# Kernel optimization log

Hardware: AMD Instinct MI355X
Metric: run time of the kernel (lower is better)

## Reference

```python
import jax, jax.numpy as jnp
import numpy as np

N_LAYERS, B, S, D, H, DH = 4, 4, 512, 512, 8, 64
MEM, CMEM, RATIO, FFMUL, VOCAB, LLAT = 512, 128, 4, 4, 512, 256
KV = CMEM + MEM + S  # 1152


def layernorm(x, g, b, eps=1e-5):
    mu = x.mean(-1, keepdims=True)
    var = ((x - mu) ** 2).mean(-1, keepdims=True)
    return (x - mu) * jax.lax.rsqrt(var + eps) * g + b


def shift(x):
    # Music-Transformer skewing: x [..., i, j] -> relative-shifted [..., i, j]
    *lead, i, j = x.shape
    x = jnp.concatenate([x, jnp.zeros((*lead, i, i), x.dtype)], -1)
    l = i + j - 1
    x = x.reshape(*lead, i * (i + j))
    pad = (-x.shape[-1]) % l
    x = jnp.concatenate([x, jnp.zeros((*lead, pad), x.dtype)], -1)
    x = x.reshape(*lead, -1, l)
    return x[..., :i, i - 1:]


def full_attn(q, k, v, mask=None, pos_emb=None):
    dh = q.shape[-1]
    dots = jnp.einsum('bhid,bhjd->bhij', q, k) * (dh ** -0.5)
    if pos_emb is not None:
        pos_dots = jnp.einsum('bhid,hjd->bhij', q, pos_emb) * (dh ** 0.5)
        pos_dots = shift(pos_dots)[..., :dots.shape[-1]]
        dots = dots + pos_dots
    if mask is not None:
        dots = jnp.where(mask, dots, jnp.asarray(-1e9, dots.dtype))
    attn = jax.nn.softmax(dots, -1)
    return jnp.einsum('bhij,bhjd->bhid', attn, v), attn


def heads(x):
    b, n, _ = x.shape
    return x.reshape(b, n, H, DH).transpose(0, 2, 1, 3)


def mha(q_in, k_in, v_in, W, mask=None, pos_emb=None):
    # W: [4, D, D] (q, k, v, out), applied as x @ W
    q, k, v = heads(q_in @ W[0]), heads(k_in @ W[1]), heads(v_in @ W[2])
    x, w = full_attn(q, k, v, mask=mask, pos_emb=pos_emb)
    x = x.transpose(0, 2, 1, 3).reshape(q_in.shape[0], -1, D)
    return x @ W[3], w


def conv_compress(mem, w, b):
    # Conv1d(D, D, RATIO, stride=RATIO): kernel==stride -> block reshape
    Bb, L, _ = mem.shape
    m = mem.reshape(Bb, L // RATIO, RATIO, D)
    return jnp.einsum('blrd,odr->blo', m, w) + b


def forward(trg, trg_mask, src_mask, latent, mems, cmems, pos_emb, embed,
            W_self, ln1_g, ln1_b, conv_w, conv_b, W_src, ln2_g, ln2_b,
            w1, b1, w2, b2):
    x = jnp.take(embed, trg, axis=0)  # [B, S, D]
    tm = trg_mask[:, :, None] & trg_mask[:, None, :]  # [B, S, S]
    tm = jnp.pad(tm, ((0, 0), (0, 0), (CMEM + MEM, 0)), constant_values=True)[:, None]  # [B,1,S,KV]
    sm = src_mask[:, None]  # [B, 1, S, LLAT]
    sg = jax.lax.stop_gradient
    attn_loss = jnp.asarray(0.0, jnp.float32)
    for i in range(N_LAYERS):
        m, cm = mems[i], cmems[i]
        kv = jnp.concatenate([cm, m, x], 1)  # [B, KV, D]
        a, _ = mha(x, kv, kv, W_self[i], mask=tm, pos_emb=pos_emb)
        a = layernorm(a + x, ln1_g[i], ln1_b[i])
        old_mem = m[:, :S]
        new_cm = conv_compress(old_mem, conv_w[i], conv_b[i])  # [B, S//RATIO, D]
        x = a
        # reconstruction attention loss: detached h / weights / old_mem
        Wq, Wk, Wv = sg(W_self[i, 0]), sg(W_self[i, 1]), sg(W_self[i, 2])
        hs = sg(x)

        def rattn(mm):
            q, k, v = heads(hs @ Wq), heads(mm @ Wk), heads(mm @ Wv)
            return full_attn(q, k, v)[0]

        target = sg(rattn(sg(old_mem)))
        attn_loss = attn_loss + jnp.mean((rattn(new_cm) - target) ** 2)
        # cross attention to latent
        x, _ = mha(x, latent, latent, W_src[i], mask=sm)
        # residual pre-norm feed-forward (GELU, exact erf as nn.GELU)
        y = layernorm(x, ln2_g[i], ln2_b[i])
        x = x + jax.nn.gelu(y @ w1[i] + b1[i], approximate=False) @ w2[i] + b2[i]
    return x, attn_loss / N_LAYERS


def setup_inputs() -> dict:
    key = jax.random.key(0)
    ks = jax.random.split(key, 16)
    sc = 0.02
    return {
        'trg': jax.random.randint(ks[0], (B, S), 0, VOCAB, dtype=jnp.int32),
        'trg_mask': jnp.ones((B, S), dtype=bool),
        'src_mask': jnp.ones((B, S, LLAT), dtype=bool),
        'latent': jax.random.normal(ks[1], (B, LLAT, D), jnp.float32),
        'mems': jax.random.normal(ks[2], (N_LAYERS, B, MEM, D), jnp.float32) * sc,
        'cmems': jax.random.normal(ks[3], (N_LAYERS, B, CMEM, D), jnp.float32) * sc,
        'pos_emb': jax.random.normal(ks[4], (H, KV, DH), jnp.float32) * sc,
        'embed': jax.random.normal(ks[5], (VOCAB, D), jnp.float32) * sc,
        'W_self': jax.random.normal(ks[6], (N_LAYERS, 4, D, D), jnp.float32) * sc,
        'ln1_g': jnp.ones((N_LAYERS, D), jnp.float32),
        'ln1_b': jnp.zeros((N_LAYERS, D), jnp.float32),
        'conv_w': jax.random.normal(ks[7], (N_LAYERS, D, D, RATIO), jnp.float32) * sc,
        'conv_b': jnp.zeros((N_LAYERS, D), jnp.float32),
        'W_src': jax.random.normal(ks[8], (N_LAYERS, 4, D, D), jnp.float32) * sc,
        'ln2_g': jnp.ones((N_LAYERS, D), jnp.float32),
        'ln2_b': jnp.zeros((N_LAYERS, D), jnp.float32),
        'w1': jax.random.normal(ks[9], (N_LAYERS, D, D * FFMUL), jnp.float32) * sc,
        'b1': jnp.zeros((N_LAYERS, D * FFMUL), jnp.float32),
        'w2': jax.random.normal(ks[10], (N_LAYERS, D * FFMUL, D), jnp.float32) * sc,
        'b2': jnp.zeros((N_LAYERS, D), jnp.float32),
    }


def reference(trg, trg_mask, src_mask, latent, mems, cmems, pos_emb, embed,
              W_self, ln1_g, ln1_b, conv_w, conv_b, W_src, ln2_g, ln2_b,
              w1, b1, w2, b2):
    return forward(trg, trg_mask, src_mask, latent, mems, cmems, pos_emb, embed,
                   W_self, ln1_g, ln1_b, conv_w, conv_b, W_src, ln2_g, ln2_b,
                   w1, b1, w2, b2)
```

## Files before the change

kernel.cpp:

```cpp
#include <hip/hip_runtime.h>
#include <math.h>

typedef float floatx4 __attribute__((ext_vector_type(4)));
typedef __bf16 bf16x8 __attribute__((ext_vector_type(8)));
typedef unsigned short u16;

#define LDK 72

__device__ inline u16 to_bf16(float f) {
  union { float f; unsigned u; } v; v.f = f;
  unsigned u = v.u;
  u += 0x7FFFu + ((u >> 16) & 1u);
  return (u16)(u >> 16);
}
__device__ inline float bf2f(u16 h) {
  union { unsigned u; float f; } v; v.u = ((unsigned)h) << 16; return v.f;
}

__device__ inline void gload16(const void* g, void* l) {
  __builtin_amdgcn_global_load_lds(
      (const __attribute__((address_space(1))) unsigned int*)g,
      (__attribute__((address_space(3))) unsigned int*)l, 16, 0, 0);
}

struct GemmArgs {
  const void* A; const void* B; void* C;
  int lda, ldb, ldc, N, Kc;
  long sA1, sA2, sB1, sB2, sC1, sC2;
  float alpha;
  const float* bias;
  const float* res; int ldres;
  const float* aml;
  int amode;
  int cmode;
  int act;
  int smode;
  int bdiv, kparts;
  int gx, gy;
};

#define MAXG 10
struct GemmBatch {
  GemmArgs g[MAXG];
  int end[MAXG];
  int ng;
};

__global__ __launch_bounds__(256) void gemmb_k(GemmBatch gb) {
  int bid = blockIdx.x;
  int gi = 0;
  while (bid >= gb.end[gi]) ++gi;
  const GemmArgs g = gb.g[gi];
  int lb = bid - (gi ? gb.end[gi - 1] : 0);
  int tid = threadIdx.x;

  if (g.amode == 8) {
    long i = (long)lb * 1024 + tid * 4;
    const float* bs = g.bias;
    int bi = (int)(i & 511);
    float4 r = *(const float4*)(g.res + i);
    float4 v;
    v.x = r.x + bs[bi]; v.y = r.y + bs[bi + 1];
    v.z = r.z + bs[bi + 2]; v.w = r.w + bs[bi + 3];
    *(float4*)((float*)g.C + i) = v;
    return;
  }
  if (g.amode == 9) {
    const float* oc = (const float*)g.A;
    const float* Op = (const float*)g.B;
    const float* ml = g.aml;
    float s = 0.f;
    for (long i = (long)lb * 256 + tid; i < 1048576; i += 256L * g.gx) {
      int row = (int)(i >> 9), col = (int)(i & 511), h = col >> 6;
      const float* mlp = ml + ((long)row * 8 + h) * 2;
      float m0v = mlp[0], l0v = mlp[1];
      float m1v = mlp[32768], l1v = mlp[32769];
      float mm = fmaxf(m0v, m1v);
      float w0 = __expf(m0v - mm), w1 = __expf(m1v - mm);
      float ov = (w0 * Op[i] + w1 * Op[1048576 + i]) / (w0 * l0v + w1 * l1v);
      float d = oc[i] - ov; s += d * d;
    }
    for (int o = 32; o > 0; o >>= 1) s += __shfl_xor(s, o, 64);
    __shared__ float red[4];
    if ((tid & 63) == 0) red[tid >> 6] = s;
    __syncthreads();
    if (tid == 0) atomicAdd((float*)g.C, red[0] + red[1] + red[2] + red[3]);
    return;
  }

  int bx = lb % g.gx;
  int rem = lb / g.gx;
  int by = rem % g.gy;
  int z = rem / g.gy;

  int kp = z % g.kparts;
  int zz = z / g.kparts;
  int zi = zz / g.bdiv, zj = zz % g.bdiv;
  long aoff = (long)zi * g.sA1 + (long)zj * g.sA2;
  long boff = (long)zi * g.sB1 + (long)zj * g.sB2;
  long coff = (long)zi * g.sC1 + (long)zj * g.sC2;
  const float* Af = (const float*)g.A + aoff;
  const u16* Ah = (const u16*)g.A + aoff;
  const u16* Bh = (const u16*)g.B + boff;

  int m0 = by * 64, n0 = bx * 64;
  __shared__ u16 As[64][64];
  __shared__ u16 Bs[64][64];
  char* Asb = (char*)&As[0][0];
  char* Bsb = (char*)&Bs[0][0];
  int wave = tid >> 6, lane = tid & 63;
  int wr = (wave >> 1) * 32, wc = (wave & 1) * 32;
  int lr = lane & 15, qrow = lane >> 4;

  unsigned o0 = wave * 1024u + lane * 16u;
  unsigned o1 = o0 + 4096u;
  int ga_r0 = o0 >> 7, ga_r1 = o1 >> 7;
  int ga_c0 = (int)(o0 & 127u) ^ ((ga_r0 & 7) << 4);
  int ga_c1 = (int)(o1 & 127u) ^ ((ga_r1 & 7) << 4);
  long ldaB = (long)g.lda * 2, ldbB = (long)g.ldb * 2;
  int r = tid >> 2, c16 = (tid & 3) << 4;
  int sw0 = (r << 7) + (((tid & 3) << 5) ^ ((r & 7) << 4));
  int sw1 = (r << 7) + ((((tid & 3) << 5) + 16) ^ ((r & 7) << 4));

  floatx4 acc[2][2];
#pragma unroll
  for (int i = 0; i < 2; ++i)
#pragma unroll
    for (int j = 0; j < 2; ++j)
#pragma unroll
      for (int rr = 0; rr < 4; ++rr) acc[i][j][rr] = 0.f;

  int kb0 = kp * g.Kc, kb1 = kb0 + g.Kc;
  for (int k0 = kb0; k0 < kb1; k0 += 64) {
    if (g.amode == 1) {
      const char* Ab = (const char*)Ah + ((long)m0 * g.lda + k0) * 2;
      gload16(Ab + ga_r0 * ldaB + ga_c0, Asb + wave * 1024);
      gload16(Ab + ga_r1 * ldaB + ga_c1, Asb + 4096 + wave * 1024);
    } else if (g.amode == 0) {
      const float* ap = Af + (long)(m0 + r) * g.lda + k0 + c16;
      float4 a0 = *(const float4*)ap, a1 = *(const float4*)(ap + 4);
      float4 a2 = *(const float4*)(ap + 8), a3 = *(const float4*)(ap + 12);
      union { u16 s[8]; uint4 v; } u0, u1;
      u0.s[0] = to_bf16(a0.x); u0.s[1] = to_bf16(a0.y); u0.s[2] = to_bf16(a0.z); u0.s[3] = to_bf16(a0.w);
      u0.s[4] = to_bf16(a1.x); u0.s[5] = to_bf16(a1.y); u0.s[6] = to_bf16(a1.z); u0.s[7] = to_bf16(a1.w);
      u1.s[0] = to_bf16(a2.x); u1.s[1] = to_bf16(a2.y); u1.s[2] = to_bf16(a2.z); u1.s[3] = to_bf16(a2.w);
      u1.s[4] = to_bf16(a3.x); u1.s[5] = to_bf16(a3.y); u1.s[6] = to_bf16(a3.z); u1.s[7] = to_bf16(a3.w);
      *(uint4*)(Asb + sw0) = u0.v; *(uint4*)(Asb + sw1) = u1.v;
    } else {
      int row = m0 + r;
      int k = k0 + c16;
      int ns = g.N;
      const float* mlp = g.aml + ((long)row * 8 + (k >> 6)) * 2;
      float mm = -1e30f;
#pragma unroll 3
      for (int s = 0; s < 3; ++s)
        if (s < ns) mm = fmaxf(mm, mlp[s * 32768]);
      float wgt[3]; float den = 0.f;
#pragma unroll 3
      for (int s = 0; s < 3; ++s)
        if (s < ns) { wgt[s] = __expf(mlp[s * 32768] - mm); den += wgt[s] * mlp[s * 32768 + 1]; }
      float inv = 1.f / den;
      float a16[16];
#pragma unroll
      for (int j = 0; j < 16; ++j) a16[j] = 0.f;
      const float* p0 = (const float*)g.A + (long)row * g.lda + k;
#pragma unroll 3
      for (int s = 0; s < 3; ++s)
        if (s < ns) {
          float w = wgt[s] * inv;
          const float* p = p0 + (long)s * g.sA1;
#pragma unroll
          for (int j = 0; j < 4; ++j) {
            float4 xx = *(const float4*)(p + j * 4);
            a16[j * 4 + 0] += w * xx.x; a16[j * 4 + 1] += w * xx.y;
            a16[j * 4 + 2] += w * xx.z; a16[j * 4 + 3] += w * xx.w;
          }
        }
      union { u16 s[8]; uint4 v; } u0, u1;
#pragma unroll
      for (int j = 0; j < 8; ++j) u0.s[j] = to_bf16(a16[j]);
#pragma unroll
      for (int j = 0; j < 8; ++j) u1.s[j] = to_bf16(a16[8 + j]);
      *(uint4*)(Asb + sw0) = u0.v; *(uint4*)(Asb + sw1) = u1.v;
    }
    {
      const char* Bb = (const char*)Bh + ((long)n0 * g.ldb + k0) * 2;
      gload16(Bb + ga_r0 * ldbB + ga_c0, Bsb + wave * 1024);
      gload16(Bb + ga_r1 * ldbB + ga_c1, Bsb + 4096 + wave * 1024);
    }
    __syncthreads();
#pragma unroll
    for (int ks = 0; ks < 2; ++ks) {
      int xk = ((ks * 32 + qrow * 8) << 1) ^ ((lr & 7) << 4);
      int rA0 = wr + lr, rB0 = wc + lr;
      bf16x8 a0 = *(const bf16x8*)(Asb + (rA0 << 7) + xk);
      bf16x8 a1 = *(const bf16x8*)(Asb + ((rA0 + 16) << 7) + xk);
      bf16x8 b0 = *(const bf16x8*)(Bsb + (rB0 << 7) + xk);
      bf16x8 b1 = *(const bf16x8*)(Bsb + ((rB0 + 16) << 7) + xk);
      acc[0][0] = __builtin_amdgcn_mfma_f32_16x16x32_bf16(a0, b0, acc[0][0], 0, 0, 0);
      acc[0][1] = __builtin_amdgcn_mfma_f32_16x16x32_bf16(a0, b1, acc[0][1], 0, 0, 0);
      acc[1][0] = __builtin_amdgcn_mfma_f32_16x16x32_bf16(a1, b0, acc[1][0], 0, 0, 0);
      acc[1][1] = __builtin_amdgcn_mfma_f32_16x16x32_bf16(a1, b1, acc[1][1], 0, 0, 0);
    }
    __syncthreads();
  }

#pragma unroll
  for (int mt = 0; mt < 2; ++mt)
#pragma unroll
    for (int nt = 0; nt < 2; ++nt) {
      int row0 = m0 + wr + mt * 16 + qrow * 4;
      int col = n0 + wc + nt * 16 + lr;
      if (g.cmode == 2) {
        ushort4 o;
        o.x = to_bf16(acc[mt][nt][0] * g.alpha);
        o.y = to_bf16(acc[mt][nt][1] * g.alpha);
        o.z = to_bf16(acc[mt][nt][2] * g.alpha);
        o.w = to_bf16(acc[mt][nt][3] * g.alpha);
        *(ushort4*)((u16*)g.C + coff + (long)col * g.ldc + row0) = o;
      } else {
#pragma unroll
        for (int rr = 0; rr < 4; ++rr) {
          int row = row0 + rr;
          float v = acc[mt][nt][rr] * g.alpha;
          if (g.cmode == 3) {
            atomicAdd((float*)g.C + coff + (long)row * g.ldc + col, v);
          } else if (g.smode) {
            int oc = col + row - 511;
            if (oc >= 0) ((u16*)g.C + coff)[(long)row * g.ldc + oc] = to_bf16(v);
          } else {
            if (g.bias) v += g.bias[col];
            if (g.res) v += g.res[(long)row * g.ldres + col];
            if (g.act) v = 0.5f * v * (1.0f + erff(v * 0.70710678118654752f));
            if (g.cmode == 1) ((u16*)g.C + coff)[(long)row * g.ldc + col] = to_bf16(v);
            else ((float*)g.C + coff)[(long)row * g.ldc + col] = v;
          }
        }
      }
    }
}

struct FAttnArgs {
  const u16* Q; const u16* K; const u16* V; const u16* QP;
  void* O; float* Opart; float* ml;
  int L, nsplit; long sKb, sVb; int ldV;
  float scale; int obf16;
};

struct FBatch {
  FAttnArgs a[3];
  int zend[3];
  int nf;
};

__global__ __launch_bounds__(256) void fattnb_k(FBatch fb) {
  int zg = blockIdx.z;
  int fi = 0;
  while (zg >= fb.zend[fi]) ++fi;
  const FAttnArgs a = fb.a[fi];
  int zl = zg - (fi ? fb.zend[fi - 1] : 0);

  int qt = blockIdx.x, h = blockIdx.y;
  int b = zl / a.nsplit, sp = zl % a.nsplit;
  int Lc = a.L / a.nsplit, kt0 = sp * Lc, T = Lc >> 6;
  int tid = threadIdx.x, wave = tid >> 6, lane = tid & 63;
  int lr = lane & 15, quad = lane >> 4;
  __shared__ u16 Qs[64][LDK];
  __shared__ u16 Ks[2][64][LDK];
  __shared__ u16 Vs[2][64][LDK];
  __shared__ u16 Qp[4][16][LDK];
  __shared__ u16 Ps[4][16][LDK];
  int r = tid >> 2, c = (tid & 3) << 4;
  {
    const u16* qp = a.Q + (long)(b * 512 + qt * 64 + r) * 512 + h * 64 + c;
    *(uint4*)&Qs[r][c] = *(const uint4*)qp;
    *(uint4*)&Qs[r][c + 8] = *(const uint4*)(qp + 8);
  }
  const u16* Kb = a.K + (long)b * a.sKb + h * 64;
  const u16* Vb = a.V + (long)b * a.sVb + (long)(h * 64) * a.ldV;
  int qrow16 = lane >> 2, qc = (lane & 3) << 4;
  const u16* QPr = a.QP ? a.QP + ((long)b * 8 + h) * 589824 +
                          (long)(qt * 64 + wave * 16 + qrow16) * 1152 : nullptr;
  {
    const u16* kp = Kb + (long)(kt0 + r) * 512 + c;
    *(uint4*)&Ks[0][r][c] = *(const uint4*)kp;
    *(uint4*)&Ks[0][r][c + 8] = *(const uint4*)(kp + 8);
    const u16* vp = Vb + (long)r * a.ldV + kt0 + c;
    *(uint4*)&Vs[0][r][c] = *(const uint4*)vp;
    *(uint4*)&Vs[0][r][c + 8] = *(const uint4*)(vp + 8);
  }
  uint4 qpr0, qpr1;
  if (QPr) {
    qpr0 = *(const uint4*)(QPr + kt0 + qc);
    qpr1 = *(const uint4*)(QPr + kt0 + qc + 8);
  }

  float m_run[4], l_run[4];
  floatx4 oacc[4];
#pragma unroll
  for (int i = 0; i < 4; ++i) {
    m_run[i] = -1e30f; l_run[i] = 0.f;
#pragma unroll
    for (int j = 0; j < 4; ++j) oacc[i][j] = 0.f;
  }

  for (int t = 0; t < T; ++t) {
    int cur = t & 1;
    bool more = (t + 1) < T;
    __syncthreads();
    uint4 pk0, pk1, pv0, pv1;
    if (more) {
      int kt = kt0 + (t + 1) * 64;
      const u16* kp = Kb + (long)(kt + r) * 512 + c;
      pk0 = *(const uint4*)kp; pk1 = *(const uint4*)(kp + 8);
      const u16* vp = Vb + (long)r * a.ldV + kt + c;
      pv0 = *(const uint4*)vp; pv1 = *(const uint4*)(vp + 8);
    }
    floatx4 sacc[4];
#pragma unroll
    for (int nt = 0; nt < 4; ++nt)
#pragma unroll
      for (int j = 0; j < 4; ++j) sacc[nt][j] = 0.f;
#pragma unroll
    for (int ks = 0; ks < 2; ++ks) {
      int kq = ks * 32 + quad * 8;
      bf16x8 av = *(const bf16x8*)&Qs[wave * 16 + lr][kq];
#pragma unroll
      for (int nt = 0; nt < 4; ++nt) {
        bf16x8 bb = *(const bf16x8*)&Ks[cur][nt * 16 + lr][kq];
        sacc[nt] = __builtin_amdgcn_mfma_f32_16x16x32_bf16(av, bb, sacc[nt], 0, 0, 0);
      }
    }
    if (QPr) {
      *(uint4*)&Qp[wave][qrow16][qc] = qpr0;
      *(uint4*)&Qp[wave][qrow16][qc + 8] = qpr1;
#pragma unroll
      for (int nt = 0; nt < 4; ++nt)
#pragma unroll
        for (int rr = 0; rr < 4; ++rr)
          sacc[nt][rr] = sacc[nt][rr] * a.scale + bf2f(Qp[wave][quad * 4 + rr][nt * 16 + lr]);
      if (more) {
        qpr0 = *(const uint4*)(QPr + kt0 + (t + 1) * 64 + qc);
        qpr1 = *(const uint4*)(QPr + kt0 + (t + 1) * 64 + qc + 8);
      }
    } else {
#pragma unroll
      for (int nt = 0; nt < 4; ++nt)
#pragma unroll
        for (int rr = 0; rr < 4; ++rr) sacc[nt][rr] *= a.scale;
    }
#pragma unroll
    for (int rr = 0; rr < 4; ++rr) {
      float m = -1e30f;
#pragma unroll
      for (int nt = 0; nt < 4; ++nt) m = fmaxf(m, sacc[nt][rr]);
      for (int o = 8; o > 0; o >>= 1) m = fmaxf(m, __shfl_xor(m, o, 64));
      float mn = fmaxf(m_run[rr], m);
      float al = __expf(m_run[rr] - mn);
      m_run[rr] = mn;
      float s = 0.f;
#pragma unroll
      for (int nt = 0; nt < 4; ++nt) {
        float p = __expf(sacc[nt][rr] - mn);
        sacc[nt][rr] = p;
        s += p;
      }
      for (int o = 8; o > 0; o >>= 1) s += __shfl_xor(s, o, 64);
      l_run[rr] = l_run[rr] * al + s;
#pragma unroll
      for (int nt = 0; nt < 4; ++nt) oacc[nt][rr] *= al;
    }
#pragma unroll
    for (int nt = 0; nt < 4; ++nt) {
      Ps[wave][quad * 4 + 0][nt * 16 + lr] = to_bf16(sacc[nt][0]);
      Ps[wave][quad * 4 + 1][nt * 16 + lr] = to_bf16(sacc[nt][1]);
      Ps[wave][quad * 4 + 2][nt * 16 + lr] = to_bf16(sacc[nt][2]);
      Ps[wave][quad * 4 + 3][nt * 16 + lr] = to_bf16(sacc[nt][3]);
    }
#pragma unroll
    for (int ks = 0; ks < 2; ++ks) {
      int kq = ks * 32 + quad * 8;
      bf16x8 av = *(const bf16x8*)&Ps[wave][lr][kq];
#pragma unroll
      for (int nt = 0; nt < 4; ++nt) {
        bf16x8 bb = *(const bf16x8*)&Vs[cur][nt * 16 + lr][kq];
        oacc[nt] = __builtin_amdgcn_mfma_f32_16x16x32_bf16(av, bb, oacc[nt], 0, 0, 0);
      }
    }
    if (more) {
      *(uint4*)&Ks[cur ^ 1][r][c] = pk0; *(uint4*)&Ks[cur ^ 1][r][c + 8] = pk1;
      *(uint4*)&Vs[cur ^ 1][r][c] = pv0; *(uint4*)&Vs[cur ^ 1][r][c + 8] = pv1;
    }
  }
  if (a.nsplit == 1) {
    float inv[4];
#pragma unroll
    for (int rr = 0; rr < 4; ++rr) inv[rr] = 1.f / l_run[rr];
#pragma unroll
    for (int nt = 0; nt < 4; ++nt)
#pragma unroll
      for (int rr = 0; rr < 4; ++rr) {
        long row = b * 512 + qt * 64 + wave * 16 + quad * 4 + rr;
        float v = oacc[nt][rr] * inv[rr];
        if (a.obf16) ((u16*)a.O)[row * 512 + h * 64 + nt * 16 + lr] = to_bf16(v);
        else ((float*)a.O)[row * 512 + h * 64 + nt * 16 + lr] = v;
      }
  } else {
#pragma unroll
    for (int nt = 0; nt < 4; ++nt)
#pragma unroll
      for (int rr = 0; rr < 4; ++rr) {
        long row = b * 512 + qt * 64 + wave * 16 + quad * 4 + rr;
        a.Opart[((long)sp * 2048 + row) * 512 + h * 64 + nt * 16 + lr] = oacc[nt][rr];
      }
    if (lr == 0)
#pragma unroll
      for (int rr = 0; rr < 4; ++rr) {
        long row = b * 512 + qt * 64 + wave * 16 + quad * 4 + rr;
        long mi = (((long)sp * 2048 + row) * 8 + h) * 2;
        a.ml[mi] = m_run[rr]; a.ml[mi + 1] = l_run[rr];
      }
  }
}

struct PrepArgs { const void* a; const void* b; void* c; int mode, p0, p1, gx, gy; };
struct PrepBatch { PrepArgs p[10]; int end[10]; int np; };

__global__ __launch_bounds__(256) void prep_k(PrepBatch pb) {
  int bid = blockIdx.x, gi = 0;
  while (bid >= pb.end[gi]) ++gi;
  PrepArgs p = pb.p[gi];
  int lb = bid - (gi ? pb.end[gi - 1] : 0);
  int tid = threadIdx.x;
  __shared__ float t[32][33];
  if (p.mode == 0) {
    int i = lb * 256 + tid;
    int row = i >> 9, d = i & 511;
    ((float*)p.c)[i] = ((const float*)p.a)[(long)((const int*)p.b)[row] * 512 + d];
  } else if (p.mode == 1) {
    int K = p.p0, N = p.p1;
    int bx = lb % p.gx, by = (lb / p.gx) % p.gy, z = lb / (p.gx * p.gy);
    const float* in = (const float*)p.a + (long)z * K * N;
    u16* out = (u16*)p.c + (long)z * K * N;
    int n0 = bx * 32, k0 = by * 32;
    int tx = tid & 31, ty = tid >> 5;
    for (int j = 0; j < 32; j += 8) t[ty + j][tx] = in[(long)(k0 + ty + j) * N + n0 + tx];
    __syncthreads();
    for (int j = 0; j < 32; j += 8) out[(long)(n0 + ty + j) * K + k0 + tx] = to_bf16(t[tx][ty + j]);
  } else if (p.mode == 2) {
    int z = lb >> 12; int i = (lb & 4095) * 256 + tid;
    int o = i >> 11, k = i & 2047, r2 = k >> 9, d = k & 511;
    ((u16*)p.c)[(long)z * 1048576 + i] =
        to_bf16(((const float*)p.a)[(long)z * 1048576 + o * 2048 + d * 4 + r2]);
  } else if (p.mode == 3) {
    int i = lb * 256 + tid;
    if (i < p.p0) ((u16*)p.c)[i] = to_bf16(((const float*)p.a)[i]);
  } else if (p.mode == 4) {
    int i = lb * 256 + tid;
    ((float*)p.c)[i] = ((const float*)p.a)[((i >> 18) << 9) + (i & 511)];
  } else {
    int i = lb * 256 + tid;
    if (i < p.p0) { uint4 z4 = {0, 0, 0, 0}; ((uint4*)p.c)[i] = z4; }
  }
}

__global__ __launch_bounds__(256) void layernorm_k(const float* __restrict__ X,
                                                   const float* __restrict__ g,
                                                   const float* __restrict__ b,
                                                   u16* __restrict__ Y) {
  long row = blockIdx.x;
  const float* x = X + row * 512;
  int tid = threadIdx.x;
  float v0 = x[tid], v1 = x[tid + 256];
  __shared__ float red[256];
  red[tid] = v0 + v1; __syncthreads();
  for (int o = 128; o > 0; o >>= 1) { if (tid < o) red[tid] += red[tid + o]; __syncthreads(); }
  float mu = red[0] * (1.f / 512.f);
  __syncthreads();
  float d0 = v0 - mu, d1 = v1 - mu;
  red[tid] = d0 * d0 + d1 * d1; __syncthreads();
  for (int o = 128; o > 0; o >>= 1) { if (tid < o) red[tid] += red[tid + o]; __syncthreads(); }
  float rstd = rsqrtf(red[0] * (1.f / 512.f) + 1e-5f);
  Y[row * 512 + tid] = to_bf16(d0 * rstd * g[tid] + b[tid]);
  Y[row * 512 + tid + 256] = to_bf16(d1 * rstd * g[tid + 256] + b[tid + 256]);
}

__global__ __launch_bounds__(256) void finalize_k(const float* __restrict__ x,
                                                  const float* __restrict__ loss,
                                                  float* __restrict__ out) {
  long i = (long)blockIdx.x * 256 + threadIdx.x;
  if (i < 1048576) out[i] = x[i];
  else if (i == 1048576) out[i] = loss[0] * (1.f / (1048576.f * 4.f));
}

extern "C" void kernel_launch(void* const* d_in, const int* in_sizes, int n_in,
                              void* d_out, int out_size, void* d_ws, size_t ws_size,
                              hipStream_t stream) {
  (void)in_sizes; (void)n_in; (void)out_size;
  const int* trg = (const int*)d_in[0];
  const float* latent = (const float*)d_in[3];
  const float* mems = (const float*)d_in[4];
  const float* cmems = (const float*)d_in[5];
  const float* pos_emb = (const float*)d_in[6];
  const float* embed = (const float*)d_in[7];
  const float* W_self = (const float*)d_in[8];
  const float* ln1_g = (const float*)d_in[9];
  const float* ln1_b = (const float*)d_in[10];
  const float* conv_w = (const float*)d_in[11];
  const float* conv_b = (const float*)d_in[12];
  const float* W_src = (const float*)d_in[13];
  const float* ln2_g = (const float*)d_in[14];
  const float* ln2_b = (const float*)d_in[15];
  const float* w1 = (const float*)d_in[16];
  const float* b1 = (const float*)d_in[17];
  const float* w2 = (const float*)d_in[18];
  const float* b2 = (const float*)d_in[19];

  float* ws = (float*)d_ws;
  long off = 0;
  auto alloc = [&](long n) { float* p = ws + off; off += (n + 63) & ~63L; return p; };
  float* x    = alloc(1048576);
  float* t0   = alloc(1048576);
  float* t1   = alloc(1048576);
  float* ocm  = alloc(1048576);
  float* Opart= alloc(3145728);
  float* mlb  = alloc(98304);
  float* Opart2 = alloc(2097152);
  u16* h1   = (u16*)Opart2;
  float* mlb2 = alloc(65536);
  u16* qb   = (u16*)alloc(524288);
  u16* qc   = (u16*)alloc(524288);
  u16* xa   = (u16*)alloc(524288);
  u16* t1h  = (u16*)alloc(524288);
  u16* kbuf = (u16*)alloc(1179648);
  u16* vbuf = (u16*)alloc(1179648);
  u16* kcm4 = (u16*)alloc(524288);
  u16* vcm4 = (u16*)alloc(524288);
  u16* klat4= (u16*)alloc(1048576);
  u16* vlat4= (u16*)alloc(1048576);
  float* ncm4 = alloc(1048576);
  u16* SQP  = (u16*)alloc(9437184);
  u16* wts  = (u16*)alloc(2097152);
  u16* wsr  = (u16*)alloc(2097152);
  u16* w1t  = (u16*)alloc(2097152);
  u16* w2t  = (u16*)alloc(2097152);
  u16* cwt  = (u16*)alloc(2097152);
  u16* post = (u16*)alloc(294912);
  float* lossacc = alloc(64);
  if ((size_t)off * 4 > ws_size) return;

  PrepBatch PB; PB.np = 0; int ptot = 0;
  auto padd = [&](int mode, const void* a, const void* b, void* c,
                  int p0, int p1, int gx, int gy, int blocks) {
    PrepArgs pa; pa.a = a; pa.b = b; pa.c = c; pa.mode = mode;
    pa.p0 = p0; pa.p1 = p1; pa.gx = gx; pa.gy = gy;
    PB.p[PB.np] = pa; ptot += blocks; PB.end[PB.np] = ptot; PB.np++;
  };
  padd(0, embed, trg, x, 0, 0, 0, 0, 4096);
  padd(1, W_self, nullptr, wts, 512, 512, 16, 16, 4096);
  padd(1, W_src, nullptr, wsr, 512, 512, 16, 16, 4096);
  padd(1, w1, nullptr, w1t, 512, 2048, 64, 16, 4096);
  padd(1, w2, nullptr, w2t, 2048, 512, 16, 64, 4096);
  padd(2, conv_w, nullptr, cwt, 0, 0, 0, 0, 16384);
  padd(3, pos_emb, nullptr, post, 589824, 0, 0, 0, 2304);
  padd(4, conv_b, nullptr, ncm4, 0, 0, 0, 0, 4096);
  padd(5, nullptr, nullptr, SQP, 2359296, 0, 0, 0, 9216);
  padd(5, nullptr, nullptr, lossacc, 1, 0, 0, 0, 1);
  prep_k<<<dim3(ptot), 256, 0, stream>>>(PB);

  auto ga = []() { GemmArgs g; g.alpha = 1.f; g.bias = nullptr; g.res = nullptr; g.ldres = 512;
                   g.aml = nullptr;
                   g.amode = 0; g.cmode = 0; g.act = 0; g.smode = 0; g.bdiv = 1; g.kparts = 1;
                   g.sA1 = g.sA2 = g.sB1 = g.sB2 = g.sC1 = g.sC2 = 0; g.N = 0;
                   g.gx = g.gy = 1; return g; };
  GemmBatch GB; GB.ng = 0; int gtot = 0;
  auto badd = [&](GemmArgs g, int gx, int gy, int gz) {
    g.gx = gx; g.gy = gy;
    GB.g[GB.ng] = g; gtot += gx * gy * gz; GB.end[GB.ng] = gtot; GB.ng++;
  };
  auto brun = [&]() {
    gemmb_k<<<dim3(gtot), 256, 0, stream>>>(GB);
    GB.ng = 0; gtot = 0;
  };
  auto run1 = [&](GemmArgs g, int gx, int gy, int gz) { badd(g, gx, gy, gz); brun(); };

  FBatch FB; FB.nf = 0; int ztot = 0;
  auto fadd = [&](const u16* Q, const u16* K, const u16* V, const u16* QP, void* O,
                  int L, int nsplit, long sKb, long sVb, int ldV, int obf16,
                  float* Op, float* ml) {
    FAttnArgs a; a.Q = Q; a.K = K; a.V = V; a.QP = QP; a.O = O;
    a.Opart = Op; a.ml = ml;
    a.L = L; a.nsplit = nsplit; a.sKb = sKb; a.sVb = sVb; a.ldV = ldV;
    a.scale = 0.125f; a.obf16 = obf16;
    FB.a[FB.nf] = a; ztot += 4 * nsplit; FB.zend[FB.nf] = ztot; FB.nf++;
  };
  auto frun = [&]() {
    fattnb_k<<<dim3(8, 8, ztot), 256, 0, stream>>>(FB);
    FB.nf = 0; ztot = 0;
  };

  { GemmArgs g = ga(); g.A = latent; g.lda = 512; g.B = wsr + 262144; g.ldb = 512;
    g.sB1 = 1048576; g.C = klat4; g.ldc = 512; g.sC1 = 524288; g.cmode = 1; g.Kc = 512;
    badd(g, 8, 16, 4); }
  { GemmArgs g = ga(); g.A = latent; g.lda = 512; g.B = wsr + 2 * 262144; g.ldb = 512;
    g.sB1 = 1048576; g.C = vlat4; g.ldc = 1024; g.sC1 = 524288; g.cmode = 2; g.Kc = 512;
    badd(g, 8, 16, 4); }
  { GemmArgs g = ga(); g.A = mems; g.lda = 2048; g.sA1 = 1048576;
    g.B = cwt; g.ldb = 2048; g.sB1 = 1048576;
    g.C = ncm4; g.ldc = 512; g.sC1 = 262144; g.cmode = 3; g.kparts = 8; g.Kc = 256;
    badd(g, 8, 8, 32); }
  brun();

  for (int l = 0; l < 4; ++l) {
    const u16* Wt0 = wts + (l * 4 + 0) * 262144;
    const u16* Wt1 = wts + (l * 4 + 1) * 262144;
    const u16* Wt2 = wts + (l * 4 + 2) * 262144;
    const u16* Wt3 = wts + (l * 4 + 3) * 262144;
    const u16* Ws0 = wsr + (l * 4 + 0) * 262144;
    const u16* Ws3 = wsr + (l * 4 + 3) * 262144;
    const float* mem_l = mems + (long)l * 1048576;
    const float* cmem_l = cmems + (long)l * 262144;
    const u16* kcm_l = kcm4 + (long)l * 262144;
    const u16* vcm_l = vcm4 + (long)l * 262144;
    const u16* klat_l = klat4 + (long)l * 524288;
    const u16* vlat_l = vlat4 + (long)l * 524288;

    { GemmArgs g = ga(); g.A = x; g.lda = 512; g.B = Wt0; g.ldb = 512; g.C = qb; g.ldc = 512;
      g.cmode = 1; g.Kc = 512; badd(g, 8, 32, 1); }
    { GemmArgs g = ga(); g.A = cmem_l; g.lda = 512; g.sA1 = 65536; g.B = Wt1; g.ldb = 512;
      g.C = kbuf; g.ldc = 512; g.sC1 = 589824; g.cmode = 1; g.Kc = 512; badd(g, 8, 2, 4); }
    { GemmArgs g = ga(); g.A = mem_l; g.lda = 512; g.sA1 = 262144; g.B = Wt1; g.ldb = 512;
      g.C = kbuf + 128 * 512; g.ldc = 512; g.sC1 = 589824; g.cmode = 1; g.Kc = 512;
      badd(g, 8, 8, 4); }
    { GemmArgs g = ga(); g.A = x; g.lda = 512; g.sA1 = 262144; g.B = Wt1; g.ldb = 512;
      g.C = kbuf + 640 * 512; g.ldc = 512; g.sC1 = 589824; g.cmode = 1; g.Kc = 512;
      badd(g, 8, 8, 4); }
    { GemmArgs g = ga(); g.A = cmem_l; g.lda = 512; g.sA1 = 65536; g.B = Wt2; g.ldb = 512;
      g.C = vbuf; g.ldc = 1152; g.sC1 = 589824; g.cmode = 2; g.Kc = 512; badd(g, 8, 2, 4); }
    { GemmArgs g = ga(); g.A = mem_l; g.lda = 512; g.sA1 = 262144; g.B = Wt2; g.ldb = 512;
      g.C = vbuf + 128; g.ldc = 1152; g.sC1 = 589824; g.cmode = 2; g.Kc = 512;
      badd(g, 8, 8, 4); }
    { GemmArgs g = ga(); g.A = x; g.lda = 512; g.sA1 = 262144; g.B = Wt2; g.ldb = 512;
      g.C = vbuf + 640; g.ldc = 1152; g.sC1 = 589824; g.cmode = 2; g.Kc = 512;
      badd(g, 8, 8, 4); }
    if (l == 0) {
      { GemmArgs g = ga(); g.A = ncm4; g.lda = 512; g.sA1 = 262144; g.B = wts + 262144;
        g.ldb = 512; g.sB1 = 1048576; g.C = kcm4; g.ldc = 512; g.sC1 = 262144;
        g.cmode = 1; g.Kc = 512; badd(g, 8, 8, 4); }
      { GemmArgs g = ga(); g.A = ncm4; g.lda = 512; g.sA1 = 262144; g.B = wts + 2 * 262144;
        g.ldb = 512; g.sB1 = 1048576; g.C = vcm4; g.ldc = 512; g.sC1 = 262144;
        g.cmode = 2; g.Kc = 512; badd(g, 8, 8, 4); }
    }
    brun();

    { GemmArgs g = ga(); g.A = qb; g.amode = 1; g.lda = 512; g.sA1 = 262144; g.sA2 = 64;
      g.B = post; g.ldb = 64; g.sB1 = 0; g.sB2 = 73728;
      g.C = SQP; g.ldc = 1152; g.sC1 = 4718592; g.sC2 = 589824;
      g.smode = 1; g.alpha = 8.f; g.bdiv = 8; g.Kc = 64; run1(g, 18, 8, 32); }

    fadd(qb, kbuf, vbuf, SQP, nullptr, 1152, 3, 589824, 589824, 1152, 1, Opart, mlb);
    frun();
    { GemmArgs g = ga(); g.A = Opart; g.amode = 2; g.N = 3; g.aml = mlb; g.lda = 512;
      g.sA1 = 1048576; g.B = Wt3; g.ldb = 512; g.C = t1; g.ldc = 512; g.res = x; g.Kc = 512;
      run1(g, 8, 32, 1); }
    layernorm_k<<<2048, 256, 0, stream>>>(t1, ln1_g + l * 512, ln1_b + l * 512, xa);

    { GemmArgs g = ga(); g.A = xa; g.amode = 1; g.lda = 512; g.B = Wt0; g.ldb = 512;
      g.C = qb; g.ldc = 512; g.cmode = 1; g.Kc = 512; badd(g, 8, 32, 1); }
    { GemmArgs g = ga(); g.A = xa; g.amode = 1; g.lda = 512; g.B = Ws0; g.ldb = 512;
      g.C = qc; g.ldc = 512; g.cmode = 1; g.Kc = 512; badd(g, 8, 32, 1); }
    brun();

    fadd(qb, kcm_l, vcm_l, nullptr, ocm, 128, 1, 65536, 128, 512, 0, Opart, mlb);
    fadd(qb, kbuf + 128 * 512, vbuf + 128, nullptr, nullptr, 512, 2, 589824, 589824, 1152, 0,
         Opart, mlb);
    fadd(qc, klat_l, vlat_l, nullptr, nullptr, 256, 2, 131072, 256, 1024, 1, Opart2, mlb2);
    frun();

    { GemmArgs g = ga(); g.A = Opart2; g.amode = 2; g.N = 2; g.aml = mlb2; g.lda = 512;
      g.sA1 = 1048576; g.B = Ws3; g.ldb = 512; g.C = t0; g.ldc = 512; g.Kc = 512;
      run1(g, 8, 32, 1); }
    layernorm_k<<<2048, 256, 0, stream>>>(t0, ln2_g + l * 512, ln2_b + l * 512, t1h);

    { GemmArgs g = ga(); g.A = t1h; g.amode = 1; g.lda = 512; g.B = w1t + (long)l * 1048576;
      g.ldb = 512; g.C = h1; g.ldc = 2048; g.cmode = 1; g.bias = b1 + l * 2048; g.act = 1;
      g.Kc = 512; badd(g, 32, 32, 1); }
    { GemmArgs g = ga(); g.amode = 9; g.A = ocm; g.B = Opart; g.aml = mlb; g.C = lossacc;
      badd(g, 128, 1, 1); }
    { GemmArgs g = ga(); g.amode = 8; g.res = t0; g.bias = b2 + l * 512; g.C = x;
      badd(g, 1024, 1, 1); }
    brun();

    { GemmArgs g = ga(); g.A = h1; g.amode = 1; g.lda = 2048; g.B = w2t + (long)l * 1048576;
      g.ldb = 2048; g.C = x; g.ldc = 512; g.cmode = 3; g.kparts = 4; g.Kc = 512;
      run1(g, 8, 32, 4); }
  }
  finalize_k<<<4097, 256, 0, stream>>>(x, lossacc, (float*)d_out);
}
```

Measured before the change: 1.134 ms.

## Pre-convert activations to bf16, drop split-K atomics, remap blocks across XCDs

Converts mems, cmems, latent and the embedded x to bf16 once in the prep kernel, and makes the FFN2 GEMM write both fp32 and bf16 copies of x. Later GEMMs can then load bf16 A operands directly instead of converting fp32. The FFN2 and conv-compress GEMMs drop split-K atomics and the separate residual-add/bias pass in favour of full-K GEMMs with a fused bias and residual epilogue. Block IDs are remapped so contiguous work lands on the same XCD. The trade-offs are fewer blocks for the full-K GEMMs, less parallelism, and extra bf16 conversion traffic up front.

```diff
diff --git a/kernel.cpp b/kernel.cpp
--- a/kernel.cpp
+++ b/kernel.cpp
@@ -24,11 +24,11 @@
 }
 
 struct GemmArgs {
-  const void* A; const void* B; void* C;
+  const void* A; const void* B; void* C; void* C2;
   int lda, ldb, ldc, N, Kc;
   long sA1, sA2, sB1, sB2, sC1, sC2;
   float alpha;
-  const float* bias;
+  const float* bias; int biasz;
   const float* res; int ldres;
   const float* aml;
   int amode;
@@ -47,24 +47,18 @@
 };
 
 __global__ __launch_bounds__(256) void gemmb_k(GemmBatch gb) {
-  int bid = blockIdx.x;
+  int nwg = gridDim.x;
+  int hw = blockIdx.x;
+  int qn = nwg >> 3, rn = nwg & 7;
+  int xcd = hw & 7, ii = hw >> 3;
+  int bid = (xcd < rn ? xcd * (qn + 1) : rn * (qn + 1) + (xcd - rn) * qn) + ii;
+
   int gi = 0;
   while (bid >= gb.end[gi]) ++gi;
   const GemmArgs g = gb.g[gi];
   int lb = bid - (gi ? gb.end[gi - 1] : 0);
   int tid = threadIdx.x;
 
-  if (g.amode == 8) {
-    long i = (long)lb * 1024 + tid * 4;
-    const float* bs = g.bias;
-    int bi = (int)(i & 511);
-    float4 r = *(const float4*)(g.res + i);
-    float4 v;
-    v.x = r.x + bs[bi]; v.y = r.y + bs[bi + 1];
-    v.z = r.z + bs[bi + 2]; v.w = r.w + bs[bi + 3];
-    *(float4*)((float*)g.C + i) = v;
-    return;
-  }
   if (g.amode == 9) {
     const float* oc = (const float*)g.A;
     const float* Op = (const float*)g.B;
@@ -229,11 +223,14 @@
             int oc = col + row - 511;
             if (oc >= 0) ((u16*)g.C + coff)[(long)row * g.ldc + oc] = to_bf16(v);
           } else {
-            if (g.bias) v += g.bias[col];
+            if (g.bias) v += g.bias[col + zi * g.biasz];
             if (g.res) v += g.res[(long)row * g.ldres + col];
             if (g.act) v = 0.5f * v * (1.0f + erff(v * 0.70710678118654752f));
             if (g.cmode == 1) ((u16*)g.C + coff)[(long)row * g.ldc + col] = to_bf16(v);
-            else ((float*)g.C + coff)[(long)row * g.ldc + col] = v;
+            else if (g.cmode == 4) {
+              ((float*)g.C + coff)[(long)row * g.ldc + col] = v;
+              ((u16*)g.C2 + coff)[(long)row * g.ldc + col] = to_bf16(v);
+            } else ((float*)g.C + coff)[(long)row * g.ldc + col] = v;
           }
         }
       }
@@ -423,8 +420,8 @@
   }
 }
 
-struct PrepArgs { const void* a; const void* b; void* c; int mode, p0, p1, gx, gy; };
-struct PrepBatch { PrepArgs p[10]; int end[10]; int np; };
+struct PrepArgs { const void* a; const void* b; void* c; void* d; int mode, p0, p1, gx, gy; };
+struct PrepBatch { PrepArgs p[12]; int end[12]; int np; };
 
 __global__ __launch_bounds__(256) void prep_k(PrepBatch pb) {
   int bid = blockIdx.x, gi = 0;
@@ -436,7 +433,9 @@
   if (p.mode == 0) {
     int i = lb * 256 + tid;
     int row = i >> 9, d = i & 511;
-    ((float*)p.c)[i] = ((const float*)p.a)[(long)((const int*)p.b)[row] * 512 + d];
+    float v = ((const float*)p.a)[(long)((const int*)p.b)[row] * 512 + d];
+    ((float*)p.c)[i] = v;
+    ((u16*)p.d)[i] = to_bf16(v);
   } else if (p.mode == 1) {
     int K = p.p0, N = p.p1;
     int bx = lb % p.gx, by = (lb / p.gx) % p.gy, z = lb / (p.gx * p.gy);
@@ -455,9 +454,6 @@
   } else if (p.mode == 3) {
     int i = lb * 256 + tid;
     if (i < p.p0) ((u16*)p.c)[i] = to_bf16(((const float*)p.a)[i]);
-  } else if (p.mode == 4) {
-    int i = lb * 256 + tid;
-    ((float*)p.c)[i] = ((const float*)p.a)[((i >> 18) << 9) + (i & 511)];
   } else {
     int i = lb * 256 + tid;
     if (i < p.p0) { uint4 z4 = {0, 0, 0, 0}; ((uint4*)p.c)[i] = z4; }
@@ -532,13 +528,17 @@
   u16* qc   = (u16*)alloc(524288);
   u16* xa   = (u16*)alloc(524288);
   u16* t1h  = (u16*)alloc(524288);
+  u16* xh   = (u16*)alloc(262144);
   u16* kbuf = (u16*)alloc(1179648);
   u16* vbuf = (u16*)alloc(1179648);
   u16* kcm4 = (u16*)alloc(524288);
   u16* vcm4 = (u16*)alloc(524288);
   u16* klat4= (u16*)alloc(1048576);
   u16* vlat4= (u16*)alloc(1048576);
-  float* ncm4 = alloc(1048576);
+  u16* ncm4h= (u16*)alloc(524288);
+  u16* memh = (u16*)alloc(2097152);
+  u16* cmemh= (u16*)alloc(524288);
+  u16* lath = (u16*)alloc(262144);
   u16* SQP  = (u16*)alloc(9437184);
   u16* wts  = (u16*)alloc(2097152);
   u16* wsr  = (u16*)alloc(2097152);
@@ -550,26 +550,28 @@
   if ((size_t)off * 4 > ws_size) return;
 
   PrepBatch PB; PB.np = 0; int ptot = 0;
-  auto padd = [&](int mode, const void* a, const void* b, void* c,
+  auto padd = [&](int mode, const void* a, const void* b, void* c, void* d,
                   int p0, int p1, int gx, int gy, int blocks) {
-    PrepArgs pa; pa.a = a; pa.b = b; pa.c = c; pa.mode = mode;
+    PrepArgs pa; pa.a = a; pa.b = b; pa.c = c; pa.d = d; pa.mode = mode;
     pa.p0 = p0; pa.p1 = p1; pa.gx = gx; pa.gy = gy;
     PB.p[PB.np] = pa; ptot += blocks; PB.end[PB.np] = ptot; PB.np++;
   };
-  padd(0, embed, trg, x, 0, 0, 0, 0, 4096);
-  padd(1, W_self, nullptr, wts, 512, 512, 16, 16, 4096);
-  padd(1, W_src, nullptr, wsr, 512, 512, 16, 16, 4096);
-  padd(1, w1, nullptr, w1t, 512, 2048, 64, 16, 4096);
-  padd(1, w2, nullptr, w2t, 2048, 512, 16, 64, 4096);
-  padd(2, conv_w, nullptr, cwt, 0, 0, 0, 0, 16384);
-  padd(3, pos_emb, nullptr, post, 589824, 0, 0, 0, 2304);
-  padd(4, conv_b, nullptr, ncm4, 0, 0, 0, 0, 4096);
-  padd(5, nullptr, nullptr, SQP, 2359296, 0, 0, 0, 9216);
-  padd(5, nullptr, nullptr, lossacc, 1, 0, 0, 0, 1);
+  padd(0, embed, trg, x, xh, 0, 0, 0, 0, 4096);
+  padd(1, W_self, nullptr, wts, nullptr, 512, 512, 16, 16, 4096);
+  padd(1, W_src, nullptr, wsr, nullptr, 512, 512, 16, 16, 4096);
+  padd(1, w1, nullptr, w1t, nullptr, 512, 2048, 64, 16, 4096);
+  padd(1, w2, nullptr, w2t, nullptr, 2048, 512, 16, 64, 4096);
+  padd(2, conv_w, nullptr, cwt, nullptr, 0, 0, 0, 0, 16384);
+  padd(3, pos_emb, nullptr, post, nullptr, 589824, 0, 0, 0, 2304);
+  padd(3, mems, nullptr, memh, nullptr, 4194304, 0, 0, 0, 16384);
+  padd(3, cmems, nullptr, cmemh, nullptr, 1048576, 0, 0, 0, 4096);
+  padd(3, latent, nullptr, lath, nullptr, 524288, 0, 0, 0, 2048);
+  padd(5, nullptr, nullptr, SQP, nullptr, 2359296, 0, 0, 0, 9216);
+  padd(5, nullptr, nullptr, lossacc, nullptr, 1, 0, 0, 0, 1);
   prep_k<<<dim3(ptot), 256, 0, stream>>>(PB);
 
-  auto ga = []() { GemmArgs g; g.alpha = 1.f; g.bias = nullptr; g.res = nullptr; g.ldres = 512;
-                   g.aml = nullptr;
+  auto ga = []() { GemmArgs g; g.alpha = 1.f; g.bias = nullptr; g.biasz = 0; g.res = nullptr;
+                   g.ldres = 512; g.aml = nullptr; g.C2 = nullptr;
                    g.amode = 0; g.cmode = 0; g.act = 0; g.smode = 0; g.bdiv = 1; g.kparts = 1;
                    g.sA1 = g.sA2 = g.sB1 = g.sB2 = g.sC1 = g.sC2 = 0; g.N = 0;
                    g.gx = g.gy = 1; return g; };
@@ -599,16 +601,17 @@
     FB.nf = 0; ztot = 0;
   };
 
-  { GemmArgs g = ga(); g.A = latent; g.lda = 512; g.B = wsr + 262144; g.ldb = 512;
+  { GemmArgs g = ga(); g.A = lath; g.amode = 1; g.lda = 512; g.B = wsr + 262144; g.ldb = 512;
     g.sB1 = 1048576; g.C = klat4; g.ldc = 512; g.sC1 = 524288; g.cmode = 1; g.Kc = 512;
     badd(g, 8, 16, 4); }
-  { GemmArgs g = ga(); g.A = latent; g.lda = 512; g.B = wsr + 2 * 262144; g.ldb = 512;
+  { GemmArgs g = ga(); g.A = lath; g.amode = 1; g.lda = 512; g.B = wsr + 2 * 262144; g.ldb = 512;
     g.sB1 = 1048576; g.C = vlat4; g.ldc = 1024; g.sC1 = 524288; g.cmode = 2; g.Kc = 512;
     badd(g, 8, 16, 4); }
-  { GemmArgs g = ga(); g.A = mems; g.lda = 2048; g.sA1 = 1048576;
+  { GemmArgs g = ga(); g.A = memh; g.amode = 1; g.lda = 2048; g.sA1 = 1048576;
     g.B = cwt; g.ldb = 2048; g.sB1 = 1048576;
-    g.C = ncm4; g.ldc = 512; g.sC1 = 262144; g.cmode = 3; g.kparts = 8; g.Kc = 256;
-    badd(g, 8, 8, 32); }
+    g.C = ncm4h; g.ldc = 512; g.sC1 = 262144; g.cmode = 1;
+    g.bias = conv_b; g.biasz = 512; g.Kc = 2048;
+    badd(g, 8, 8, 4); }
   brun();
 
   for (int l = 0; l < 4; ++l) {
@@ -618,38 +621,44 @@
     const u16* Wt3 = wts + (l * 4 + 3) * 262144;
     const u16* Ws0 = wsr + (l * 4 + 0) * 262144;
     const u16* Ws3 = wsr + (l * 4 + 3) * 262144;
-    const float* mem_l = mems + (long)l * 1048576;
-    const float* cmem_l = cmems + (long)l * 262144;
+    const u16* memh_l = memh + (long)l * 1048576;
+    const u16* cmemh_l = cmemh + (long)l * 262144;
     const u16* kcm_l = kcm4 + (long)l * 262144;
     const u16* vcm_l = vcm4 + (long)l * 262144;
     const u16* klat_l = klat4 + (long)l * 524288;
     const u16* vlat_l = vlat4 + (long)l * 524288;
 
-    { GemmArgs g = ga(); g.A = x; g.lda = 512; g.B = Wt0; g.ldb = 512; g.C = qb; g.ldc = 512;
-      g.cmode = 1; g.Kc = 512; badd(g, 8, 32, 1); }
-    { GemmArgs g = ga(); g.A = cmem_l; g.lda = 512; g.sA1 = 65536; g.B = Wt1; g.ldb = 512;
+    { GemmArgs g = ga(); g.A = xh; g.amode = 1; g.lda = 512; g.B = Wt0; g.ldb = 512;
+      g.C = qb; g.ldc = 512; g.cmode = 1; g.Kc = 512; badd(g, 8, 32, 1); }
+    { GemmArgs g = ga(); g.A = cmemh_l; g.amode = 1; g.lda = 512; g.sA1 = 65536;
+      g.B = Wt1; g.ldb = 512;
       g.C = kbuf; g.ldc = 512; g.sC1 = 589824; g.cmode = 1; g.Kc = 512; badd(g, 8, 2, 4); }
-    { GemmArgs g = ga(); g.A = mem_l; g.lda = 512; g.sA1 = 262144; g.B = Wt1; g.ldb = 512;
+    { GemmArgs g = ga(); g.A = memh_l; g.amode = 1; g.lda = 512; g.sA1 = 262144;
+      g.B = Wt1; g.ldb = 512;
       g.C = kbuf + 128 * 512; g.ldc = 512; g.sC1 = 589824; g.cmode = 1; g.Kc = 512;
       badd(g, 8, 8, 4); }
-    { GemmArgs g = ga(); g.A = x; g.lda = 512; g.sA1 = 262144; g.B = Wt1; g.ldb = 512;
+    { GemmArgs g = ga(); g.A = xh; g.amode = 1; g.lda = 512; g.sA1 = 262144;
+      g.B = Wt1; g.ldb = 512;
       g.C = kbuf + 640 * 512; g.ldc = 512; g.sC1 = 589824; g.cmode = 1; g.Kc = 512;
       badd(g, 8, 8, 4); }
-    { GemmArgs g = ga(); g.A = cmem_l; g.lda = 512; g.sA1 = 65536; g.B = Wt2; g.ldb = 512;
+    { GemmArgs g = ga(); g.A = cmemh_l; g.amode = 1; g.lda = 512; g.sA1 = 65536;
+      g.B = Wt2; g.ldb = 512;
       g.C = vbuf; g.ldc = 1152; g.sC1 = 589824; g.cmode = 2; g.Kc = 512; badd(g, 8, 2, 4); }
-    { GemmArgs g = ga(); g.A = mem_l; g.lda = 512; g.sA1 = 262144; g.B = Wt2; g.ldb = 512;
+    { GemmArgs g = ga(); g.A = memh_l; g.amode = 1; g.lda = 512; g.sA1 = 262144;
+      g.B = Wt2; g.ldb = 512;
       g.C = vbuf + 128; g.ldc = 1152; g.sC1 = 589824; g.cmode = 2; g.Kc = 512;
       badd(g, 8, 8, 4); }
-    { GemmArgs g = ga(); g.A = x; g.lda = 512; g.sA1 = 262144; g.B = Wt2; g.ldb = 512;
+    { GemmArgs g = ga(); g.A = xh; g.amode = 1; g.lda = 512; g.sA1 = 262144;
+      g.B = Wt2; g.ldb = 512;
       g.C = vbuf + 640; g.ldc = 1152; g.sC1 = 589824; g.cmode = 2; g.Kc = 512;
       badd(g, 8, 8, 4); }
     if (l == 0) {
-      { GemmArgs g = ga(); g.A = ncm4; g.lda = 512; g.sA1 = 262144; g.B = wts + 262144;
-        g.ldb = 512; g.sB1 = 1048576; g.C = kcm4; g.ldc = 512; g.sC1 = 262144;
-        g.cmode = 1; g.Kc = 512; badd(g, 8, 8, 4); }
-      { GemmArgs g = ga(); g.A = ncm4; g.lda = 512; g.sA1 = 262144; g.B = wts + 2 * 262144;
-        g.ldb = 512; g.sB1 = 1048576; g.C = vcm4; g.ldc = 512; g.sC1 = 262144;
-        g.cmode = 2; g.Kc = 512; badd(g, 8, 8, 4); }
+      { GemmArgs g = ga(); g.A = ncm4h; g.amode = 1; g.lda = 512; g.sA1 = 262144;
+        g.B = wts + 262144; g.ldb = 512; g.sB1 = 1048576;
+        g.C = kcm4; g.ldc = 512; g.sC1 = 262144; g.cmode = 1; g.Kc = 512; badd(g, 8, 8, 4); }
+      { GemmArgs g = ga(); g.A = ncm4h; g.amode = 1; g.lda = 512; g.sA1 = 262144;
+        g.B = wts + 2 * 262144; g.ldb = 512; g.sB1 = 1048576;
+        g.C = vcm4; g.ldc = 512; g.sC1 = 262144; g.cmode = 2; g.Kc = 512; badd(g, 8, 8, 4); }
     }
     brun();
 
@@ -687,13 +696,13 @@
       g.Kc = 512; badd(g, 32, 32, 1); }
     { GemmArgs g = ga(); g.amode = 9; g.A = ocm; g.B = Opart; g.aml = mlb; g.C = lossacc;
       badd(g, 128, 1, 1); }
-    { GemmArgs g = ga(); g.amode = 8; g.res = t0; g.bias = b2 + l * 512; g.C = x;
-      badd(g, 1024, 1, 1); }
     brun();
 
-    { GemmArgs g = ga(); g.A = h1; g.amode = 1; g.lda = 2048; g.B = w2t + (long)l * 1048576;
-      g.ldb = 2048; g.C = x; g.ldc = 512; g.cmode = 3; g.kparts = 4; g.Kc = 512;
-      run1(g, 8, 32, 4); }
+    { GemmArgs g = ga(); g.A = h1; g.amode = 1; g.lda = 2048;
+      g.B = w2t + (long)l * 1048576; g.ldb = 2048;
+      g.C = x; g.C2 = xh; g.ldc = 512; g.cmode = 4;
+      g.bias = b2 + l * 512; g.res = t0; g.Kc = 2048;
+      run1(g, 8, 32, 1); }
   }
   finalize_k<<<4097, 256, 0, stream>>>(x, lossacc, (float*)d_out);
 }
```

After: 1.116 ms. Within noise of the previous version (-1.5%).
